# Optimization experiments

Measured on AMD Instinct MI355X. Metric: run time of the kernel, lower is better.

## Reference

```python
import jax, jax.numpy as jnp
import numpy as np

N_NODES = 50000
HIDDEN = 128
IN_DIM = 128
N_EDGES = 1600000


def gcn_conv(x, W, b, src, dst, deg_isqrt, n_nodes):
    # x: [N, Fin], W: [Fin, Fout]. src/dst include self-loops.
    h = x @ W  # [N, Fout]
    norm = deg_isqrt[src] * deg_isqrt[dst]  # [E+N]
    msgs = h[src] * norm[:, None]  # [E+N, Fout]
    agg = jax.ops.segment_sum(msgs, dst, num_segments=n_nodes)
    return agg + b


def setup_inputs() -> dict:
    key = jax.random.key(0)
    ks = jax.random.split(key, 8)
    x = jax.random.normal(ks[0], (N_NODES, IN_DIM), dtype=jnp.float32)
    edge_index = jax.random.randint(ks[1], (2, N_EDGES), 0, N_NODES, dtype=jnp.int64 if jax.config.jax_enable_x64 else jnp.int32)
    s1 = 1.0 / np.sqrt(IN_DIM)
    s2 = 1.0 / np.sqrt(HIDDEN)
    W1 = jax.random.uniform(ks[2], (IN_DIM, HIDDEN), jnp.float32, -s1, s1)
    b1 = jnp.zeros((HIDDEN,), jnp.float32)
    W2 = jax.random.uniform(ks[3], (HIDDEN, HIDDEN), jnp.float32, -s2, s2)
    b2 = jnp.zeros((HIDDEN,), jnp.float32)
    Wc = jax.random.uniform(ks[4], (HIDDEN, 1), jnp.float32, -s2, s2)
    bc = jnp.zeros((1,), jnp.float32)
    return {"x": x, "edge_index": edge_index, "W1": W1, "b1": b1,
            "W2": W2, "b2": b2, "Wc": Wc, "bc": bc}


def reference(x, edge_index, W1, b1, W2, b2, Wc, bc):
    n = x.shape[0]
    # add self-loops (PyG GCNConv default)
    loop = jnp.arange(n, dtype=edge_index.dtype)
    src = jnp.concatenate([edge_index[0], loop])
    dst = jnp.concatenate([edge_index[1], loop])
    # symmetric normalization: deg over augmented dst, edge weight 1
    deg = jax.ops.segment_sum(jnp.ones_like(dst, dtype=x.dtype), dst, num_segments=n)
    deg_isqrt = jnp.where(deg > 0, jax.lax.rsqrt(deg), 0.0)
    h = jax.nn.relu(gcn_conv(x, W1, b1, src, dst, deg_isqrt, n))
    h = jax.nn.relu(gcn_conv(h, W2, b2, src, dst, deg_isqrt, n))
    return (h @ Wc + bc).squeeze(-1)  # [N]
```

## Files before the change

kernel.cpp:

```cpp
#include <hip/hip_runtime.h>
#include <hip/hip_fp16.h>
#include <cstdint>


#define EPBH 4096
#define DCAP 9216

__global__ __launch_bounds__(256) void bucket_hist(const int* __restrict__ dst,
                                                   int* __restrict__ hist,
                                                   int ne, int nb, int nbuck) {
  __shared__ int lh[256];
  lh[threadIdx.x] = 0;
  __syncthreads();
  int base = blockIdx.x * EPBH;
#pragma unroll
  for (int j = 0; j < 16; ++j) {
    int e = base + j * 256 + threadIdx.x;
    if (e < ne) {
      int d = __builtin_nontemporal_load(&dst[e]);
      atomicAdd(&lh[d >> 8], 1);
    }
  }
  __syncthreads();
  if (threadIdx.x < nbuck)
    hist[(size_t)threadIdx.x * nb + blockIdx.x] = lh[threadIdx.x];
}

__global__ void scan_block(const int* __restrict__ in, int* __restrict__ part,
                           int* __restrict__ bsum, int n) {
  __shared__ int s[1024];
  int i = blockIdx.x * 1024 + threadIdx.x;
  int v = (i < n) ? in[i] : 0;
  s[threadIdx.x] = v;
  __syncthreads();
  for (int off = 1; off < 1024; off <<= 1) {
    int t = (threadIdx.x >= (unsigned)off) ? s[threadIdx.x - off] : 0;
    __syncthreads();
    s[threadIdx.x] += t;
    __syncthreads();
  }
  if (i < n) part[i] = s[threadIdx.x] - v;
  if (threadIdx.x == 1023) bsum[blockIdx.x] = s[1023];
}

__global__ void scan_partials(int* __restrict__ bsum, int nb) {
  __shared__ int s[256];
  int v = (threadIdx.x < (unsigned)nb) ? bsum[threadIdx.x] : 0;
  s[threadIdx.x] = v;
  __syncthreads();
  for (int off = 1; off < 256; off <<= 1) {
    int t = (threadIdx.x >= (unsigned)off) ? s[threadIdx.x - off] : 0;
    __syncthreads();
    s[threadIdx.x] += t;
    __syncthreads();
  }
  if (threadIdx.x < (unsigned)nb) bsum[threadIdx.x] = s[threadIdx.x] - v;
}

__global__ void finalize_scan(const int* __restrict__ part, const int* __restrict__ bsum,
                              int* __restrict__ out, int n) {
  int i = blockIdx.x * blockDim.x + threadIdx.x;
  if (i < n) out[i] = part[i] + bsum[i >> 10];
}

__global__ __launch_bounds__(256) void bucket_scatter(const int* __restrict__ src,
                                                      const int* __restrict__ dst,
                                                      const int* __restrict__ scanned,
                                                      uint2* __restrict__ ebuf,
                                                      int ne, int nb, int nbuck) {
  __shared__ int cur[256];
  if (threadIdx.x < nbuck)
    cur[threadIdx.x] = scanned[(size_t)threadIdx.x * nb + blockIdx.x];
  __syncthreads();
  int base = blockIdx.x * EPBH;
#pragma unroll
  for (int j = 0; j < 16; ++j) {
    int e = base + j * 256 + threadIdx.x;
    if (e < ne) {
      int s = __builtin_nontemporal_load(&src[e]);
      int d = __builtin_nontemporal_load(&dst[e]);
      int pos = atomicAdd(&cur[d >> 8], 1);
      ebuf[pos] = make_uint2((unsigned)s, (unsigned)d);
    }
  }
}

__global__ __launch_bounds__(256) void bucket_csr(const uint2* __restrict__ ebuf,
                                                  const int* __restrict__ scanned,
                                                  int* __restrict__ row_ptr,
                                                  float* __restrict__ dinv,
                                                  int* __restrict__ col,
                                                  int ne, int nb, int nbuck, int n) {
  __shared__ int lcnt[256];
  __shared__ int lofs[256];
  __shared__ int cur[256];
  __shared__ uint2 sbuf[DCAP];
  int b = blockIdx.x;
  int start = scanned[(size_t)b * nb];
  int end = (b + 1 < nbuck) ? scanned[(size_t)(b + 1) * nb] : ne;
  lcnt[threadIdx.x] = 0;
  __syncthreads();
  for (int k = start + threadIdx.x; k < end; k += 256) {
    uint2 ed = ebuf[k];
    int rel = k - start;
    if (rel < DCAP) sbuf[rel] = ed;
    atomicAdd(&lcnt[ed.y & 255], 1);
  }
  __syncthreads();
  int v = lcnt[threadIdx.x];
  lofs[threadIdx.x] = v;
  __syncthreads();
  for (int off = 1; off < 256; off <<= 1) {
    int t = (threadIdx.x >= (unsigned)off) ? lofs[threadIdx.x - off] : 0;
    __syncthreads();
    lofs[threadIdx.x] += t;
    __syncthreads();
  }
  int excl = lofs[threadIdx.x] - v;
  int node = b * 256 + threadIdx.x;
  if (node < n) {
    row_ptr[node] = start + excl;
    dinv[node] = rsqrtf((float)(v + 1));
  }
  cur[threadIdx.x] = start + excl;
  __syncthreads();
  for (int k = start + threadIdx.x; k < end; k += 256) {
    int rel = k - start;
    uint2 ed = (rel < DCAP) ? sbuf[rel] : ebuf[k];
    int pos = atomicAdd(&cur[ed.y & 255], 1);
    col[pos] = (int)ed.x;
  }
  if (b == nbuck - 1 && threadIdx.x == 0) row_ptr[n] = ne;
}


__global__ __launch_bounds__(256) void gemm_scale_h(const float* __restrict__ in,
                                                    const float* __restrict__ W,
                                                    const float* __restrict__ dinv,
                                                    __half* __restrict__ out, int nrows) {
  __shared__ float ws[16][128];
  __shared__ float xs[64][17];
  int row0 = blockIdx.x * 64;
  int tid = threadIdx.x;
  int rg = tid >> 4;
  int cg = tid & 15;

  float acc[4][8] = {{0.f}};

  for (int k0 = 0; k0 < 128; k0 += 16) {
    {
      int idx = tid * 8;
      int kk = idx >> 7;
      int f = idx & 127;
      float4 a = *(const float4*)&W[(size_t)(k0 + kk) * 128 + f];
      float4 b = *(const float4*)&W[(size_t)(k0 + kk) * 128 + f + 4];
      *(float4*)&ws[kk][f] = a;
      *(float4*)&ws[kk][f + 4] = b;
    }
    {
      int idx = tid * 4;
      int r = idx >> 4;
      int kk = idx & 15;
      int grow = row0 + r;
      float4 v = make_float4(0.f, 0.f, 0.f, 0.f);
      if (grow < nrows) v = *(const float4*)&in[(size_t)grow * 128 + k0 + kk];
      xs[r][kk] = v.x; xs[r][kk + 1] = v.y; xs[r][kk + 2] = v.z; xs[r][kk + 3] = v.w;
    }
    __syncthreads();
#pragma unroll
    for (int kk = 0; kk < 16; ++kk) {
      float b0[8];
      *(float4*)&b0[0] = *(const float4*)&ws[kk][cg * 4];
      *(float4*)&b0[4] = *(const float4*)&ws[kk][64 + cg * 4];
      float a0 = xs[rg * 4 + 0][kk];
      float a1 = xs[rg * 4 + 1][kk];
      float a2 = xs[rg * 4 + 2][kk];
      float a3 = xs[rg * 4 + 3][kk];
#pragma unroll
      for (int j = 0; j < 8; ++j) {
        acc[0][j] += a0 * b0[j];
        acc[1][j] += a1 * b0[j];
        acc[2][j] += a2 * b0[j];
        acc[3][j] += a3 * b0[j];
      }
    }
    __syncthreads();
  }

#pragma unroll
  for (int r = 0; r < 4; ++r) {
    int grow = row0 + rg * 4 + r;
    if (grow < nrows) {
      float s = dinv[grow];
      __half h[8];
#pragma unroll
      for (int j = 0; j < 8; ++j) h[j] = __float2half_rn(acc[r][j] * s);
      *(uint2*)&out[(size_t)grow * 128 + cg * 4] = *(uint2*)&h[0];
      *(uint2*)&out[(size_t)grow * 128 + 64 + cg * 4] = *(uint2*)&h[4];
    }
  }
}


__device__ inline float4 h4_to_f4(uint2 u) {
  __half2 a = *(__half2*)&u.x;
  __half2 b = *(__half2*)&u.y;
  float2 fa = __half22float2(a);
  float2 fb = __half22float2(b);
  return make_float4(fa.x, fa.y, fb.x, fb.y);
}


__global__ __launch_bounds__(256) void aggregate_h(const __half* __restrict__ hsh,
                                                   const int* __restrict__ row_ptr,
                                                   const int* __restrict__ col,
                                                   const float* __restrict__ dinv,
                                                   const float* __restrict__ bias,
                                                   float* __restrict__ out, int n) {
  int node = (blockIdx.x * blockDim.x + threadIdx.x) >> 6;
  if (node >= n) return;
  int lane = threadIdx.x & 63;
  int half_ = lane >> 5;
  int f4 = lane & 31;
  const uint2* rows = (const uint2*)hsh;

  int start = row_ptr[node];
  int end = row_ptr[node + 1];

  float4 acc = make_float4(0.f, 0.f, 0.f, 0.f);
  if (half_ == 0) acc = h4_to_f4(rows[(size_t)node * 32 + f4]);

  int e = start + half_;
  for (; e + 14 < end; e += 16) {
    uint2 u[8];
#pragma unroll
    for (int j = 0; j < 8; ++j) u[j] = rows[(size_t)col[e + 2 * j] * 32 + f4];
#pragma unroll
    for (int j = 0; j < 8; ++j) {
      float4 v = h4_to_f4(u[j]);
      acc.x += v.x; acc.y += v.y; acc.z += v.z; acc.w += v.w;
    }
  }
  for (; e < end; e += 2) {
    float4 v = h4_to_f4(rows[(size_t)col[e] * 32 + f4]);
    acc.x += v.x; acc.y += v.y; acc.z += v.z; acc.w += v.w;
  }

  acc.x += __shfl_xor(acc.x, 32);
  acc.y += __shfl_xor(acc.y, 32);
  acc.z += __shfl_xor(acc.z, 32);
  acc.w += __shfl_xor(acc.w, 32);

  if (half_ == 0) {
    float d = dinv[node];
    float4 b = ((const float4*)bias)[f4];
    float4 o;
    o.x = fmaxf(acc.x * d + b.x, 0.f);
    o.y = fmaxf(acc.y * d + b.y, 0.f);
    o.z = fmaxf(acc.z * d + b.z, 0.f);
    o.w = fmaxf(acc.w * d + b.w, 0.f);
    ((float4*)out)[(size_t)node * 32 + f4] = o;
  }
}


__global__ __launch_bounds__(256) void aggregate_dot_h(const __half* __restrict__ hsh,
                                                       const int* __restrict__ row_ptr,
                                                       const int* __restrict__ col,
                                                       const float* __restrict__ dinv,
                                                       const float* __restrict__ bias,
                                                       const float* __restrict__ Wc,
                                                       const float* __restrict__ bc,
                                                       float* __restrict__ out, int n) {
  int node = (blockIdx.x * blockDim.x + threadIdx.x) >> 6;
  if (node >= n) return;
  int lane = threadIdx.x & 63;
  int half_ = lane >> 5;
  int f4 = lane & 31;
  const uint2* rows = (const uint2*)hsh;

  int start = row_ptr[node];
  int end = row_ptr[node + 1];

  float4 acc = make_float4(0.f, 0.f, 0.f, 0.f);
  if (half_ == 0) acc = h4_to_f4(rows[(size_t)node * 32 + f4]);

  int e = start + half_;
  for (; e + 14 < end; e += 16) {
    uint2 u[8];
#pragma unroll
    for (int j = 0; j < 8; ++j) u[j] = rows[(size_t)col[e + 2 * j] * 32 + f4];
#pragma unroll
    for (int j = 0; j < 8; ++j) {
      float4 v = h4_to_f4(u[j]);
      acc.x += v.x; acc.y += v.y; acc.z += v.z; acc.w += v.w;
    }
  }
  for (; e < end; e += 2) {
    float4 v = h4_to_f4(rows[(size_t)col[e] * 32 + f4]);
    acc.x += v.x; acc.y += v.y; acc.z += v.z; acc.w += v.w;
  }

  acc.x += __shfl_xor(acc.x, 32);
  acc.y += __shfl_xor(acc.y, 32);
  acc.z += __shfl_xor(acc.z, 32);
  acc.w += __shfl_xor(acc.w, 32);

  float d = dinv[node];
  float4 b = ((const float4*)bias)[f4];
  float4 w = ((const float4*)Wc)[f4];
  float s = fmaxf(acc.x * d + b.x, 0.f) * w.x
          + fmaxf(acc.y * d + b.y, 0.f) * w.y
          + fmaxf(acc.z * d + b.z, 0.f) * w.z
          + fmaxf(acc.w * d + b.w, 0.f) * w.w;
#pragma unroll
  for (int off = 16; off; off >>= 1) s += __shfl_xor(s, off);
  if (lane == 0) out[node] = s + bc[0];
}


extern "C" void kernel_launch(void* const* d_in, const int* in_sizes, int n_in,
                              void* d_out, int out_size, void* d_ws, size_t ws_size,
                              hipStream_t stream) {
  const float* x  = (const float*)d_in[0];
  const int* ei   = (const int*)d_in[1];
  const float* W1 = (const float*)d_in[2];
  const float* b1 = (const float*)d_in[3];
  const float* W2 = (const float*)d_in[4];
  const float* b2 = (const float*)d_in[5];
  const float* Wc = (const float*)d_in[6];
  const float* bc = (const float*)d_in[7];
  float* out = (float*)d_out;

  int n  = in_sizes[0] / 128;
  int ne = in_sizes[1] / 2;
  const int* src = ei;
  const int* dst = ei + ne;

  int NBb = (ne + EPBH - 1) / EPBH;
  int NBUCK = (n + 255) >> 8;
  int HN = NBUCK * NBb;

  char* p = (char*)d_ws;
  auto alloc = [&](size_t bytes) {
    char* r = p;
    p += (bytes + 255) & ~(size_t)255;
    return r;
  };
  int*    hist    = (int*)alloc((size_t)HN * 4);
  int*    part    = (int*)alloc((size_t)HN * 4);
  int*    bsum    = (int*)alloc(256 * 4);
  int*    row_ptr = (int*)alloc((size_t)(n + 1) * 4);
  float*  dinv    = (float*)alloc((size_t)n * 4);
  int*    col     = (int*)alloc((size_t)ne * 4);
  __half* hsh     = (__half*)alloc((size_t)n * 128 * 2);
  float*  h1      = (float*)alloc((size_t)n * 128 * 4);
  uint2*  ebuf    = (uint2*)h1;

  bucket_hist<<<NBb, 256, 0, stream>>>(dst, hist, ne, NBb, NBUCK);
  int nsb = (HN + 1023) / 1024;
  scan_block<<<nsb, 1024, 0, stream>>>(hist, part, bsum, HN);
  scan_partials<<<1, 256, 0, stream>>>(bsum, nsb);
  finalize_scan<<<(HN + 255) / 256, 256, 0, stream>>>(part, bsum, hist, HN);
  bucket_scatter<<<NBb, 256, 0, stream>>>(src, dst, hist, ebuf, ne, NBb, NBUCK);
  bucket_csr<<<NBUCK, 256, 0, stream>>>(ebuf, hist, row_ptr, dinv, col, ne, NBb, NBUCK, n);

  int gemm_blocks = (n + 63) / 64;
  int agg_blocks = (n + 3) / 4;

  gemm_scale_h<<<gemm_blocks, 256, 0, stream>>>(x, W1, dinv, hsh, n);
  aggregate_h<<<agg_blocks, 256, 0, stream>>>(hsh, row_ptr, col, dinv, b1, h1, n);
  gemm_scale_h<<<gemm_blocks, 256, 0, stream>>>(h1, W2, dinv, hsh, n);
  aggregate_dot_h<<<agg_blocks, 256, 0, stream>>>(hsh, row_ptr, col, dinv, b2, Wc, bc, out, n);
}
```

Baseline: 229.2 us.

## Split fp16 features into four column slabs and aggregate in per-slab passes

Result: slower. 387.8 us (+69.2%).

```diff
diff --git a/kernel.cpp b/kernel.cpp
--- a/kernel.cpp
+++ b/kernel.cpp
@@ -187,135 +187,151 @@
     __syncthreads();
   }
 
+  int c0 = cg * 4;
+  int c1 = 64 + cg * 4;
 #pragma unroll
   for (int r = 0; r < 4; ++r) {
     int grow = row0 + rg * 4 + r;
     if (grow < nrows) {
-      float s = dinv[grow];
+      float sc = dinv[grow];
       __half h[8];
 #pragma unroll
-      for (int j = 0; j < 8; ++j) h[j] = __float2half_rn(acc[r][j] * s);
-      *(uint2*)&out[(size_t)grow * 128 + cg * 4] = *(uint2*)&h[0];
-      *(uint2*)&out[(size_t)grow * 128 + 64 + cg * 4] = *(uint2*)&h[4];
-    }
-  }
-}
-
-
-__device__ inline float4 h4_to_f4(uint2 u) {
-  __half2 a = *(__half2*)&u.x;
-  __half2 b = *(__half2*)&u.y;
-  float2 fa = __half22float2(a);
-  float2 fb = __half22float2(b);
-  return make_float4(fa.x, fa.y, fb.x, fb.y);
-}
-
-
-__global__ __launch_bounds__(256) void aggregate_h(const __half* __restrict__ hsh,
-                                                   const int* __restrict__ row_ptr,
-                                                   const int* __restrict__ col,
-                                                   const float* __restrict__ dinv,
-                                                   const float* __restrict__ bias,
-                                                   float* __restrict__ out, int n) {
+      for (int j = 0; j < 8; ++j) h[j] = __float2half_rn(acc[r][j] * sc);
+      *(uint2*)&out[((size_t)(c0 >> 5) * nrows + grow) * 32 + (c0 & 31)] = *(uint2*)&h[0];
+      *(uint2*)&out[((size_t)(c1 >> 5) * nrows + grow) * 32 + (c1 & 31)] = *(uint2*)&h[4];
+    }
+  }
+}
+
+
+__global__ __launch_bounds__(256) void aggregate_pass_h(const __half* __restrict__ hsh4,
+                                                        const int* __restrict__ row_ptr,
+                                                        const int* __restrict__ col,
+                                                        const float* __restrict__ dinv,
+                                                        const float* __restrict__ bias,
+                                                        float* __restrict__ out,
+                                                        int n, int s) {
   int node = (blockIdx.x * blockDim.x + threadIdx.x) >> 6;
   if (node >= n) return;
   int lane = threadIdx.x & 63;
-  int half_ = lane >> 5;
-  int f4 = lane & 31;
-  const uint2* rows = (const uint2*)hsh;
+  int e4 = lane >> 4;
+  int f = lane & 15;
+  const uint* base = (const uint*)hsh4 + (size_t)s * n * 16;
 
   int start = row_ptr[node];
   int end = row_ptr[node + 1];
 
-  float4 acc = make_float4(0.f, 0.f, 0.f, 0.f);
-  if (half_ == 0) acc = h4_to_f4(rows[(size_t)node * 32 + f4]);
-
-  int e = start + half_;
-  for (; e + 14 < end; e += 16) {
-    uint2 u[8];
-#pragma unroll
-    for (int j = 0; j < 8; ++j) u[j] = rows[(size_t)col[e + 2 * j] * 32 + f4];
-#pragma unroll
-    for (int j = 0; j < 8; ++j) {
-      float4 v = h4_to_f4(u[j]);
-      acc.x += v.x; acc.y += v.y; acc.z += v.z; acc.w += v.w;
-    }
-  }
-  for (; e < end; e += 2) {
-    float4 v = h4_to_f4(rows[(size_t)col[e] * 32 + f4]);
-    acc.x += v.x; acc.y += v.y; acc.z += v.z; acc.w += v.w;
-  }
-
+  float2 acc = make_float2(0.f, 0.f);
+  if (e4 == 0) {
+    uint u = base[(size_t)node * 16 + f];
+    acc = __half22float2(*(__half2*)&u);
+  }
+
+  int e = start;
+  for (; e + 15 < end; e += 16) {
+    int c = __builtin_nontemporal_load(&col[e + f]);
+#pragma unroll
+    for (int j = 0; j < 4; ++j) {
+      int sn = __shfl(c, 4 * j + e4);
+      uint u = base[(size_t)sn * 16 + f];
+      float2 v = __half22float2(*(__half2*)&u);
+      acc.x += v.x; acc.y += v.y;
+    }
+  }
+  for (; e < end; e += 4) {
+    int idx = e + e4;
+    if (idx < end) {
+      int sn = __builtin_nontemporal_load(&col[idx]);
+      uint u = base[(size_t)sn * 16 + f];
+      float2 v = __half22float2(*(__half2*)&u);
+      acc.x += v.x; acc.y += v.y;
+    }
+  }
+
+  acc.x += __shfl_xor(acc.x, 16);
+  acc.y += __shfl_xor(acc.y, 16);
   acc.x += __shfl_xor(acc.x, 32);
   acc.y += __shfl_xor(acc.y, 32);
-  acc.z += __shfl_xor(acc.z, 32);
-  acc.w += __shfl_xor(acc.w, 32);
-
-  if (half_ == 0) {
+
+  if (e4 == 0) {
     float d = dinv[node];
-    float4 b = ((const float4*)bias)[f4];
-    float4 o;
-    o.x = fmaxf(acc.x * d + b.x, 0.f);
-    o.y = fmaxf(acc.y * d + b.y, 0.f);
-    o.z = fmaxf(acc.z * d + b.z, 0.f);
-    o.w = fmaxf(acc.w * d + b.w, 0.f);
-    ((float4*)out)[(size_t)node * 32 + f4] = o;
-  }
-}
-
-
-__global__ __launch_bounds__(256) void aggregate_dot_h(const __half* __restrict__ hsh,
-                                                       const int* __restrict__ row_ptr,
-                                                       const int* __restrict__ col,
-                                                       const float* __restrict__ dinv,
-                                                       const float* __restrict__ bias,
-                                                       const float* __restrict__ Wc,
-                                                       const float* __restrict__ bc,
-                                                       float* __restrict__ out, int n) {
+    float2 b = *(const float2*)&bias[s * 32 + 2 * f];
+    float* op = &out[(size_t)node * 128 + s * 32 + 2 * f];
+    __builtin_nontemporal_store(fmaxf(acc.x * d + b.x, 0.f), op);
+    __builtin_nontemporal_store(fmaxf(acc.y * d + b.y, 0.f), op + 1);
+  }
+}
+
+
+__global__ __launch_bounds__(256) void aggregate_dot_pass_h(const __half* __restrict__ hsh4,
+                                                            const int* __restrict__ row_ptr,
+                                                            const int* __restrict__ col,
+                                                            const float* __restrict__ dinv,
+                                                            const float* __restrict__ bias,
+                                                            const float* __restrict__ Wc,
+                                                            float* __restrict__ partial,
+                                                            int n, int s) {
   int node = (blockIdx.x * blockDim.x + threadIdx.x) >> 6;
   if (node >= n) return;
   int lane = threadIdx.x & 63;
-  int half_ = lane >> 5;
-  int f4 = lane & 31;
-  const uint2* rows = (const uint2*)hsh;
+  int e4 = lane >> 4;
+  int f = lane & 15;
+  const uint* base = (const uint*)hsh4 + (size_t)s * n * 16;
 
   int start = row_ptr[node];
   int end = row_ptr[node + 1];
 
-  float4 acc = make_float4(0.f, 0.f, 0.f, 0.f);
-  if (half_ == 0) acc = h4_to_f4(rows[(size_t)node * 32 + f4]);
-
-  int e = start + half_;
-  for (; e + 14 < end; e += 16) {
-    uint2 u[8];
-#pragma unroll
-    for (int j = 0; j < 8; ++j) u[j] = rows[(size_t)col[e + 2 * j] * 32 + f4];
-#pragma unroll
-    for (int j = 0; j < 8; ++j) {
-      float4 v = h4_to_f4(u[j]);
-      acc.x += v.x; acc.y += v.y; acc.z += v.z; acc.w += v.w;
-    }
-  }
-  for (; e < end; e += 2) {
-    float4 v = h4_to_f4(rows[(size_t)col[e] * 32 + f4]);
-    acc.x += v.x; acc.y += v.y; acc.z += v.z; acc.w += v.w;
-  }
-
+  float2 acc = make_float2(0.f, 0.f);
+  if (e4 == 0) {
+    uint u = base[(size_t)node * 16 + f];
+    acc = __half22float2(*(__half2*)&u);
+  }
+
+  int e = start;
+  for (; e + 15 < end; e += 16) {
+    int c = __builtin_nontemporal_load(&col[e + f]);
+#pragma unroll
+    for (int j = 0; j < 4; ++j) {
+      int sn = __shfl(c, 4 * j + e4);
+      uint u = base[(size_t)sn * 16 + f];
+      float2 v = __half22float2(*(__half2*)&u);
+      acc.x += v.x; acc.y += v.y;
+    }
+  }
+  for (; e < end; e += 4) {
+    int idx = e + e4;
+    if (idx < end) {
+      int sn = __builtin_nontemporal_load(&col[idx]);
+      uint u = base[(size_t)sn * 16 + f];
+      float2 v = __half22float2(*(__half2*)&u);
+      acc.x += v.x; acc.y += v.y;
+    }
+  }
+
+  acc.x += __shfl_xor(acc.x, 16);
+  acc.y += __shfl_xor(acc.y, 16);
   acc.x += __shfl_xor(acc.x, 32);
   acc.y += __shfl_xor(acc.y, 32);
-  acc.z += __shfl_xor(acc.z, 32);
-  acc.w += __shfl_xor(acc.w, 32);
-
-  float d = dinv[node];
-  float4 b = ((const float4*)bias)[f4];
-  float4 w = ((const float4*)Wc)[f4];
-  float s = fmaxf(acc.x * d + b.x, 0.f) * w.x
-          + fmaxf(acc.y * d + b.y, 0.f) * w.y
-          + fmaxf(acc.z * d + b.z, 0.f) * w.z
-          + fmaxf(acc.w * d + b.w, 0.f) * w.w;
-#pragma unroll
-  for (int off = 16; off; off >>= 1) s += __shfl_xor(s, off);
-  if (lane == 0) out[node] = s + bc[0];
+
+  if (e4 == 0) {
+    float d = dinv[node];
+    float2 b = *(const float2*)&bias[s * 32 + 2 * f];
+    float2 w = *(const float2*)&Wc[s * 32 + 2 * f];
+    float p = fmaxf(acc.x * d + b.x, 0.f) * w.x + fmaxf(acc.y * d + b.y, 0.f) * w.y;
+    p += __shfl_xor(p, 1);
+    p += __shfl_xor(p, 2);
+    p += __shfl_xor(p, 4);
+    p += __shfl_xor(p, 8);
+    if (f == 0) __builtin_nontemporal_store(p, &partial[(size_t)s * n + node]);
+  }
+}
+
+__global__ void reduce_out(const float* __restrict__ partial, const float* __restrict__ bc,
+                           float* __restrict__ out, int n) {
+  int i = blockIdx.x * blockDim.x + threadIdx.x;
+  if (i < n)
+    out[i] = partial[i] + partial[(size_t)n + i] + partial[2 * (size_t)n + i] +
+             partial[3 * (size_t)n + i] + bc[0];
 }
 
 
@@ -353,7 +369,8 @@
   int*    row_ptr = (int*)alloc((size_t)(n + 1) * 4);
   float*  dinv    = (float*)alloc((size_t)n * 4);
   int*    col     = (int*)alloc((size_t)ne * 4);
-  __half* hsh     = (__half*)alloc((size_t)n * 128 * 2);
+  float*  partial = (float*)alloc((size_t)n * 4 * 4);
+  __half* hsh4    = (__half*)alloc((size_t)n * 128 * 2);
   float*  h1      = (float*)alloc((size_t)n * 128 * 4);
   uint2*  ebuf    = (uint2*)h1;
 
@@ -368,8 +385,12 @@
   int gemm_blocks = (n + 63) / 64;
   int agg_blocks = (n + 3) / 4;
 
-  gemm_scale_h<<<gemm_blocks, 256, 0, stream>>>(x, W1, dinv, hsh, n);
-  aggregate_h<<<agg_blocks, 256, 0, stream>>>(hsh, row_ptr, col, dinv, b1, h1, n);
-  gemm_scale_h<<<gemm_blocks, 256, 0, stream>>>(h1, W2, dinv, hsh, n);
-  aggregate_dot_h<<<agg_blocks, 256, 0, stream>>>(hsh, row_ptr, col, dinv, b2, Wc, bc, out, n);
-}
+  gemm_scale_h<<<gemm_blocks, 256, 0, stream>>>(x, W1, dinv, hsh4, n);
+  for (int s = 0; s < 4; ++s)
+    aggregate_pass_h<<<agg_blocks, 256, 0, stream>>>(hsh4, row_ptr, col, dinv, b1, h1, n, s);
+  gemm_scale_h<<<gemm_blocks, 256, 0, stream>>>(h1, W2, dinv, hsh4, n);
+  for (int s = 0; s < 4; ++s)
+    aggregate_dot_pass_h<<<agg_blocks, 256, 0, stream>>>(hsh4, row_ptr, col, dinv, b2, Wc,
+                                                         partial, n, s);
+  reduce_out<<<(n + 255) / 256, 256, 0, stream>>>(partial, bc, out, n);
+}
```

## Replace scalar FP32 GEMM with FP16 MFMA matrix-core GEMM

Applied to the files above, without the earlier changes.

Measured after the change: 226.4 us, median of 2. No clear change (-1.2%).

```diff
diff --git a/kernel.cpp b/kernel.cpp
--- a/kernel.cpp
+++ b/kernel.cpp
@@ -134,70 +134,78 @@
 }
 
 
-__global__ __launch_bounds__(256) void gemm_scale_h(const float* __restrict__ in,
-                                                    const float* __restrict__ W,
-                                                    const float* __restrict__ dinv,
-                                                    __half* __restrict__ out, int nrows) {
-  __shared__ float ws[16][128];
-  __shared__ float xs[64][17];
+typedef _Float16 half_t;
+typedef __attribute__((ext_vector_type(8))) _Float16 f16x8;
+typedef __attribute__((ext_vector_type(4))) float f32x4;
+
+#define LDP 136
+
+__global__ __launch_bounds__(256) void gemm_mfma_h(const float* __restrict__ in,
+                                                   const float* __restrict__ W,
+                                                   const float* __restrict__ dinv,
+                                                   __half* __restrict__ out, int nrows) {
+  __shared__ half_t As[64][LDP];
+  __shared__ half_t Bs[128][LDP];
+  int tid = threadIdx.x;
   int row0 = blockIdx.x * 64;
-  int tid = threadIdx.x;
-  int rg = tid >> 4;
-  int cg = tid & 15;
-
-  float acc[4][8] = {{0.f}};
-
-  for (int k0 = 0; k0 < 128; k0 += 16) {
-    {
-      int idx = tid * 8;
-      int kk = idx >> 7;
-      int f = idx & 127;
-      float4 a = *(const float4*)&W[(size_t)(k0 + kk) * 128 + f];
-      float4 b = *(const float4*)&W[(size_t)(k0 + kk) * 128 + f + 4];
-      *(float4*)&ws[kk][f] = a;
-      *(float4*)&ws[kk][f + 4] = b;
-    }
-    {
-      int idx = tid * 4;
-      int r = idx >> 4;
-      int kk = idx & 15;
-      int grow = row0 + r;
-      float4 v = make_float4(0.f, 0.f, 0.f, 0.f);
-      if (grow < nrows) v = *(const float4*)&in[(size_t)grow * 128 + k0 + kk];
-      xs[r][kk] = v.x; xs[r][kk + 1] = v.y; xs[r][kk + 2] = v.z; xs[r][kk + 3] = v.w;
-    }
-    __syncthreads();
-#pragma unroll
-    for (int kk = 0; kk < 16; ++kk) {
-      float b0[8];
-      *(float4*)&b0[0] = *(const float4*)&ws[kk][cg * 4];
-      *(float4*)&b0[4] = *(const float4*)&ws[kk][64 + cg * 4];
-      float a0 = xs[rg * 4 + 0][kk];
-      float a1 = xs[rg * 4 + 1][kk];
-      float a2 = xs[rg * 4 + 2][kk];
-      float a3 = xs[rg * 4 + 3][kk];
-#pragma unroll
-      for (int j = 0; j < 8; ++j) {
-        acc[0][j] += a0 * b0[j];
-        acc[1][j] += a1 * b0[j];
-        acc[2][j] += a2 * b0[j];
-        acc[3][j] += a3 * b0[j];
-      }
-    }
-    __syncthreads();
-  }
-
-#pragma unroll
-  for (int r = 0; r < 4; ++r) {
-    int grow = row0 + rg * 4 + r;
-    if (grow < nrows) {
-      float s = dinv[grow];
-      __half h[8];
-#pragma unroll
-      for (int j = 0; j < 8; ++j) h[j] = __float2half_rn(acc[r][j] * s);
-      *(uint2*)&out[(size_t)grow * 128 + cg * 4] = *(uint2*)&h[0];
-      *(uint2*)&out[(size_t)grow * 128 + 64 + cg * 4] = *(uint2*)&h[4];
-    }
+
+#pragma unroll
+  for (int it = 0; it < 16; ++it) {
+    int idx = it * 256 + tid;
+    int k = idx >> 5;
+    int f4 = (idx & 31) * 4;
+    float4 w = *(const float4*)&W[(size_t)k * 128 + f4];
+    Bs[f4 + 0][k] = (half_t)w.x;
+    Bs[f4 + 1][k] = (half_t)w.y;
+    Bs[f4 + 2][k] = (half_t)w.z;
+    Bs[f4 + 3][k] = (half_t)w.w;
+  }
+#pragma unroll
+  for (int it = 0; it < 8; ++it) {
+    int idx = it * 256 + tid;
+    int r = idx >> 5;
+    int k4 = (idx & 31) * 4;
+    int grow = row0 + r;
+    float4 v = make_float4(0.f, 0.f, 0.f, 0.f);
+    if (grow < nrows) v = *(const float4*)&in[(size_t)grow * 128 + k4];
+    As[r][k4 + 0] = (half_t)v.x;
+    As[r][k4 + 1] = (half_t)v.y;
+    As[r][k4 + 2] = (half_t)v.z;
+    As[r][k4 + 3] = (half_t)v.w;
+  }
+  __syncthreads();
+
+  int wv = tid >> 6;
+  int lane = tid & 63;
+  int m = lane & 15;
+  int kg = lane >> 4;
+
+  f32x4 acc[8];
+#pragma unroll
+  for (int ct = 0; ct < 8; ++ct) acc[ct] = (f32x4){0.f, 0.f, 0.f, 0.f};
+
+#pragma unroll
+  for (int ks = 0; ks < 4; ++ks) {
+    f16x8 a = *(const f16x8*)&As[wv * 16 + m][ks * 32 + kg * 8];
+#pragma unroll
+    for (int ct = 0; ct < 8; ++ct) {
+      f16x8 b = *(const f16x8*)&Bs[ct * 16 + m][ks * 32 + kg * 8];
+      acc[ct] = __builtin_amdgcn_mfma_f32_16x16x32_f16(a, b, acc[ct], 0, 0, 0);
+    }
+  }
+
+  int orow = row0 + wv * 16 + kg * 4;
+  float d0 = (orow + 0 < nrows) ? dinv[orow + 0] : 0.f;
+  float d1 = (orow + 1 < nrows) ? dinv[orow + 1] : 0.f;
+  float d2 = (orow + 2 < nrows) ? dinv[orow + 2] : 0.f;
+  float d3 = (orow + 3 < nrows) ? dinv[orow + 3] : 0.f;
+#pragma unroll
+  for (int ct = 0; ct < 8; ++ct) {
+    int ocol = ct * 16 + m;
+    if (orow + 0 < nrows) out[(size_t)(orow + 0) * 128 + ocol] = __float2half_rn(acc[ct][0] * d0);
+    if (orow + 1 < nrows) out[(size_t)(orow + 1) * 128 + ocol] = __float2half_rn(acc[ct][1] * d1);
+    if (orow + 2 < nrows) out[(size_t)(orow + 2) * 128 + ocol] = __float2half_rn(acc[ct][2] * d2);
+    if (orow + 3 < nrows) out[(size_t)(orow + 3) * 128 + ocol] = __float2half_rn(acc[ct][3] * d3);
   }
 }
 
@@ -368,8 +376,8 @@
   int gemm_blocks = (n + 63) / 64;
   int agg_blocks = (n + 3) / 4;
 
-  gemm_scale_h<<<gemm_blocks, 256, 0, stream>>>(x, W1, dinv, hsh, n);
+  gemm_mfma_h<<<gemm_blocks, 256, 0, stream>>>(x, W1, dinv, hsh, n);
   aggregate_h<<<agg_blocks, 256, 0, stream>>>(hsh, row_ptr, col, dinv, b1, h1, n);
-  gemm_scale_h<<<gemm_blocks, 256, 0, stream>>>(h1, W2, dinv, hsh, n);
+  gemm_mfma_h<<<gemm_blocks, 256, 0, stream>>>(h1, W2, dinv, hsh, n);
   aggregate_dot_h<<<agg_blocks, 256, 0, stream>>>(hsh, row_ptr, col, dinv, b2, Wc, bc, out, n);
 }
```
